# Performance work log

Hardware: AMD Instinct MI355X
Metric: run time of the kernel (lower is better)

## Reference

```python
import jax, jax.numpy as jnp
import numpy as np
from jax import lax

T, B, D_IN, D_DAY, H, D_OUT = 64, 32, 4096, 256, 256, 942


def setup_inputs() -> dict:
    key = jax.random.key(0)
    ks = jax.random.split(key, 18)
    s = 0.05
    def rn(k, shape):
        return jax.random.normal(k, shape, jnp.float32) * s
    return {
        "x": jax.random.uniform(ks[0], (T, B, D_IN), jnp.float32),
        "W_emb": rn(ks[1], (D_DAY, D_IN)), "b_emb": rn(ks[2], (D_DAY,)),
        "Wih_f": rn(ks[3], (3 * H, D_DAY)), "Whh_f": rn(ks[4], (3 * H, H)),
        "bih_f": rn(ks[5], (3 * H,)), "bhh_f": rn(ks[6], (3 * H,)),
        "Wih_r": rn(ks[7], (3 * H, D_DAY)), "Whh_r": rn(ks[8], (3 * H, H)),
        "bih_r": rn(ks[9], (3 * H,)), "bhh_r": rn(ks[10], (3 * H,)),
        "attn_w": rn(ks[11], (2 * H,)), "attn_b": rn(ks[12], ()),
        "W_ao": rn(ks[13], (D_DAY, 4 * H)), "b_ao": rn(ks[14], (D_DAY,)),
        "W_o": rn(ks[15], (D_OUT, D_DAY)), "b_o": rn(ks[16], (D_OUT,)),
    }


def _gru_cell(xt, h, Wih, Whh, bih, bhh):
    # PyTorch nn.GRU cell math
    gi = xt @ Wih.T + bih          # [B, 3H]
    gh = h @ Whh.T + bhh           # [B, 3H]
    ir, iz, inn = jnp.split(gi, 3, axis=-1)
    hr, hz, hn = jnp.split(gh, 3, axis=-1)
    r = jax.nn.sigmoid(ir + hr)
    z = jax.nn.sigmoid(iz + hz)
    n = jnp.tanh(inn + r * hn)
    return (1.0 - z) * n + z * h


def _run_gru(seq, Wih, Whh, bih, bhh):
    # seq: [L, B, D] -> all hidden states [L, B, H], h0 = zeros
    h0 = jnp.zeros((seq.shape[1], H), seq.dtype)
    def step(h, xt):
        h2 = _gru_cell(xt, h, Wih, Whh, bih, bhh)
        return h2, h2
    return lax.scan(step, h0, seq)[1]


def reference(x, W_emb, b_emb, Wih_f, Whh_f, bih_f, bhh_f,
              Wih_r, Whh_r, bih_r, bhh_r, attn_w, attn_b,
              W_ao, b_ao, W_o, b_o):
    day_emb = jnp.einsum('tbi,di->tbd', x, W_emb) + b_emb       # [T,B,Dday]

    # Forward GRU over the prefix [:i+1] equals the first i+1 states of one full run.
    fwd = _run_gru(day_emb, Wih_f, Whh_f, bih_f, bhh_f)          # [T,B,H]

    # Reverse GRU is recomputed per timestep on the flipped prefix (O(T^2)).
    i_idx = jnp.arange(T)
    j_idx = jnp.arange(T)
    gather = jnp.clip(i_idx[:, None] - j_idx[None, :], 0)        # [T,T]
    rev_in = day_emb[gather]                                     # [T,T,B,Dday]; row i, step j = day_emb[i-j]
    rev = jax.vmap(lambda s: _run_gru(s, Wih_r, Whh_r, bih_r, bhh_r))(rev_in)  # [T,T,B,H]

    # Attention scores on concat(fwd, rev) without materializing the 2H concat:
    w_f, w_r = attn_w[:H], attn_w[H:]
    scores = (jnp.einsum('tbh,h->tb', fwd, w_f)[None, :, :]
              + jnp.einsum('itbh,h->itb', rev, w_r) + attn_b)    # [T(i),T(t),B]
    valid = j_idx[None, :] <= i_idx[:, None]                     # t <= i
    scores = jnp.where(valid[:, :, None], scores, -jnp.inf)
    alpha = jax.nn.softmax(scores, axis=1)                       # softmax over prefix time

    counts = (i_idx + 1).astype(day_emb.dtype)[:, None, None]    # mean over i+1 steps
    c_fwd = jnp.einsum('itb,tbh->ibh', alpha, fwd) / counts      # [T,B,H]
    c_rev = jnp.einsum('itb,itbh->ibh', alpha, rev) / counts     # [T,B,H]
    rev_last = rev[i_idx, i_idx]                                 # rnn_h[-1] reverse half, [T,B,H]

    h_t = jnp.concatenate([c_fwd, c_rev, fwd, rev_last], axis=-1)  # [T,B,4H]
    h_t_out = h_t @ W_ao.T + b_ao                                # [T,B,Dday]
    return jax.nn.sigmoid(h_t_out @ W_o.T + b_o)                 # [T,B,D_OUT]
```

## Files before the change

kernel.cpp:

```cpp
#include <hip/hip_runtime.h>
#include <hip/hip_bf16.h>


typedef __bf16 bf16x8 __attribute__((ext_vector_type(8)));
typedef __bf16 bf16x4 __attribute__((ext_vector_type(4)));
typedef float  f32x4  __attribute__((ext_vector_type(4)));
typedef int    int4v  __attribute__((ext_vector_type(4)));

static constexpr float NEG_L2E = -1.442695041f;
static constexpr float TWO_L2E =  2.885390082f;

static constexpr size_t OFF_PK_EMB = 0;
static constexpr size_t OFF_PK_IH  = 2097152;
static constexpr size_t OFF_WQ     = 2883584;
static constexpr size_t OFF_WSC    = 3276800;
static constexpr size_t OFF_PK_AO  = 3670016;
static constexpr size_t OFF_PK_O   = 4194304;
static constexpr size_t OFF_DAY    = 4685824;
static constexpr size_t OFF_GIT    = 5734400;
static constexpr size_t OFF_BC     = 12025856;
static constexpr size_t OFF_REV    = 18317312;
static constexpr size_t OFF_FWD    = 52396032;
static constexpr size_t OFF_HT     = 53444608;
static constexpr size_t OFF_TMP1   = 57638912;
static constexpr size_t OFF_XB     = OFF_REV;

__device__ __forceinline__ float sigf(float x) {
    return __builtin_amdgcn_rcpf(1.f + __expf(-x));
}

#define LDS_BARRIER() asm volatile("s_waitcnt lgkmcnt(0)\n\ts_barrier" ::: "memory")

__global__ __launch_bounds__(256) void pack_misc(
    const float* __restrict__ We,  const float* __restrict__ Wir, const float* __restrict__ Wif,
    const float* __restrict__ Wao, const float* __restrict__ Wo,  const float* __restrict__ x,
    __bf16* pe, __bf16* pi, __bf16* pao, __bf16* po, __bf16* xb)
{
    int b = blockIdx.x;
    if (b >= 952) {
        size_t base = ((size_t)(b - 952) * 256 + threadIdx.x) * 8;
        float4 v0 = *(const float4*)(x + base);
        float4 v1 = *(const float4*)(x + base + 4);
        bf16x8 o;
        o[0]=(__bf16)v0.x; o[1]=(__bf16)v0.y; o[2]=(__bf16)v0.z; o[3]=(__bf16)v0.w;
        o[4]=(__bf16)v1.x; o[5]=(__bf16)v1.y; o[6]=(__bf16)v1.z; o[7]=(__bf16)v1.w;
        *(bf16x8*)(xb + base) = o;
        return;
    }
    const float* src; __bf16* dst; int Nsrc, k32l, b0; bool ih = false;
    if (b < 512)      { src = We;  dst = pe;          Nsrc = 256; k32l = 7; b0 = 0;   }
    else if (b < 608) { src = Wir; dst = pi;          Nsrc = 768; k32l = 3; b0 = 512; ih = true; }
    else if (b < 704) { src = Wif; dst = pi + 196608; Nsrc = 768; k32l = 3; b0 = 608; ih = true; }
    else if (b < 832) { src = Wao; dst = pao;         Nsrc = 256; k32l = 5; b0 = 704; }
    else              { src = Wo;  dst = po;          Nsrc = 942; k32l = 3; b0 = 832; }
    int t8   = (b - b0) * 256 + threadIdx.x;
    int lane = t8 & 63;
    int K32  = 1 << k32l;
    int K    = K32 << 5;
    int ks   = (t8 >> 6) & (K32 - 1);
    int nt   = t8 >> (6 + k32l);
    int n    = nt * 16 + (lane & 15);
    int k0   = ks * 32 + ((lane >> 4) << 3);
    bf16x8 o;
    if (n < Nsrc) {
        const float* sp = src + (size_t)n * K + k0;
        float4 v0 = *(const float4*)sp;
        float4 v1 = *(const float4*)(sp + 4);
        float s = ih ? ((n < 512) ? NEG_L2E : TWO_L2E) : 1.f;
        o[0]=(__bf16)(v0.x*s); o[1]=(__bf16)(v0.y*s); o[2]=(__bf16)(v0.z*s); o[3]=(__bf16)(v0.w*s);
        o[4]=(__bf16)(v1.x*s); o[5]=(__bf16)(v1.y*s); o[6]=(__bf16)(v1.z*s); o[7]=(__bf16)(v1.w*s);
    } else {
#pragma unroll
        for (int q = 0; q < 8; q++) o[q] = (__bf16)0.f;
    }
    *(bf16x8*)(dst + (size_t)t8 * 8) = o;
}

__global__ __launch_bounds__(64) void pack_hh_i8(
    const float* __restrict__ Whr, const float* __restrict__ Whf,
    const float* __restrict__ bih_r, const float* __restrict__ bih_f,
    const float* __restrict__ bhh_r, const float* __restrict__ bhh_f,
    signed char* __restrict__ wq, float* __restrict__ wscale, float* __restrict__ bc)
{
    int b = blockIdx.x;
    int dir = (b >= 768) ? 1 : 0;
    int n = b - dir * 768;
    const float* src = (dir ? Whf : Whr) + (size_t)n * 256;
    int t = threadIdx.x;
    float4 wv = ((const float4*)src)[t];
    float m = fmaxf(fmaxf(fabsf(wv.x), fabsf(wv.y)), fmaxf(fabsf(wv.z), fabsf(wv.w)));
#pragma unroll
    for (int off = 32; off > 0; off >>= 1) m = fmaxf(m, __shfl_xor(m, off));
    m = fmaxf(m, 1e-20f);
    float inv = 127.f / m;
    int q0 = (int)__builtin_rintf(wv.x * inv);
    int q1 = (int)__builtin_rintf(wv.y * inv);
    int q2 = (int)__builtin_rintf(wv.z * inv);
    int q3 = (int)__builtin_rintf(wv.w * inv);
    int pk = (q0 & 0xff) | ((q1 & 0xff) << 8) | ((q2 & 0xff) << 16) | ((q3 & 0xff) << 24);
    int dlane = (n & 15) | (((t >> 2) & 3) << 4);
    size_t byte = (size_t)dir * 196608 + ((size_t)(n >> 4) * 4 + (t >> 4)) * 1024
                + (size_t)dlane * 16 + (t & 3) * 4;
    *(int*)(wq + byte) = pk;
    if (t == 0) {
        float gc = (n < 512) ? NEG_L2E : TWO_L2E;
        wscale[b] = m * (1.f / 16129.f) * gc;
        const float* bi = dir ? bih_f : bih_r;
        const float* bh = dir ? bhh_f : bhh_r;
        bc[b] = (n < 512) ? (bi[n] + bh[n]) * NEG_L2E : bi[n] * TWO_L2E;
    }
}

template<int MODE, int KDIM, int NTILES, int MR, int CSTRIDE, int NREAL>
__global__ __launch_bounds__(256) void gemm_k(
    const __bf16* __restrict__ Ap, const __bf16* __restrict__ Bp, void* __restrict__ Cp,
    const float* __restrict__ bias)
{
    __shared__ __align__(16) __bf16 As[MR][88];
    const int tid = threadIdx.x;
    const int w = tid >> 6, lane = tid & 63, c = lane & 15, quad = lane >> 4;
    const int mb = blockIdx.x, nb = blockIdx.y;
    constexpr int K32 = KDIM / 32;
    constexpr int NK  = KDIM / 64;
    constexpr int NT_W = (MR == 64) ? NTILES : NTILES / 2;
    constexpr int TPR  = (MR == 64) ? 4 : 8;
    constexpr int EPT  = 64 / TPR;
    const int wrow  = (MR == 64) ? w : (w & 1);
    const int ncol0 = (MR == 64) ? 0 : (w >> 1) * NT_W;

    f32x4 acc[NT_W];
#pragma unroll
    for (int nt = 0; nt < NT_W; nt++) acc[nt] = (f32x4){0.f, 0.f, 0.f, 0.f};

    const int row = tid / TPR, kp = (tid % TPR) * EPT;
    uint4 pb[EPT / 8];

    auto issue = [&](int kb) {
        const __bf16* ap = Ap + (size_t)(mb * MR + row) * KDIM + kb * 64 + kp;
        pb[0] = ((const uint4*)ap)[0];
        if constexpr (EPT == 16) pb[1] = ((const uint4*)ap)[1];
    };
    auto commit = [&]() {
        *(uint4*)&As[row][kp] = pb[0];
        if constexpr (EPT == 16) *(uint4*)&As[row][kp + 8] = pb[1];
    };

    issue(0);
    for (int kb = 0; kb < NK; kb++) {
        commit();
        __syncthreads();
        if (kb + 1 < NK) issue(kb + 1);
#pragma unroll
        for (int kk = 0; kk < 2; kk++) {
            bf16x8 a = *(const bf16x8*)&As[wrow * 16 + c][kk * 32 + quad * 8];
#pragma unroll
            for (int nt = 0; nt < NT_W; nt++) {
                bf16x8 bfr = *(const bf16x8*)(Bp +
                    ((size_t)((nb * NTILES + ncol0 + nt) * K32 + kb * 2 + kk) * 64 + lane) * 8);
                acc[nt] = __builtin_amdgcn_mfma_f32_16x16x32_bf16(a, bfr, acc[nt], 0, 0, 0);
            }
        }
        __syncthreads();
    }

    if constexpr (MODE == 1) {
        static_assert(MR == 64 && NTILES == 4, "MODE1 epilogue requires 64x64 tile");
#pragma unroll
        for (int nt = 0; nt < 4; nt++) {
            float bv = bias[nb * 64 + nt * 16 + c];
#pragma unroll
            for (int r0 = 0; r0 < 4; r0++)
                As[nt * 16 + c][w * 16 + quad * 4 + r0] = (__bf16)(acc[nt][r0] + bv);
        }
        __syncthreads();
        const int dd = tid >> 2, bch = tid & 3;
        const int n = nb * 64 + dd;
        const int dir = (n >= 768) ? 1 : 0;
        const int rem = n - dir * 768;
        const int g = rem >> 8, dcol = rem & 255;
#pragma unroll
        for (int tl = 0; tl < 2; tl++) {
            uint4 v = *(const uint4*)&As[dd][tl * 32 + bch * 8];
            size_t off = (size_t)dir * 1572864 + (size_t)(mb * 2 + tl) * 24576
                       + ((size_t)((g * 2 + (bch >> 1)) * 256 + dcol)) * 16 + (bch & 1) * 8;
            *(uint4*)((__bf16*)Cp + off) = v;
        }
    } else {
#pragma unroll
        for (int nt = 0; nt < NT_W; nt++) {
            int n = nb * (NTILES * 16) + (ncol0 + nt) * 16 + c;
            float bv = (n < NREAL) ? bias[n] : 0.f;
#pragma unroll
            for (int r0 = 0; r0 < 4; r0++) {
                int m = mb * MR + wrow * 16 + quad * 4 + r0;
                float v = acc[nt][r0] + bv;
                if constexpr (MODE == 2) ((__bf16*)Cp)[(size_t)m * CSTRIDE + n] = (__bf16)v;
                else { if (n < NREAL) ((float*)Cp)[(size_t)m * CSTRIDE + n] = sigf(v); }
            }
        }
    }
}

__global__ __launch_bounds__(1024, 4) void gru_recurrent(
    const signed char* __restrict__ wq, const float* __restrict__ wscale,
    const float* __restrict__ bhh_r, const float* __restrict__ bhh_f,
    const __bf16* __restrict__ Git,
    __bf16* __restrict__ revb, __bf16* __restrict__ fwdb)
{
    __shared__ __align__(16) signed char hbuf[2][16][272];
    __shared__ __align__(16) __bf16 hist[8][4096];
    const int tid = threadIdx.x;
    const int w = tid >> 6, lane = tid & 63, c = lane & 15, quad = lane >> 4;
    const int bid = blockIdx.x;
    const bool isF = (bid < 2);
    const int ia = isF ? 63 : (63 - ((bid - 2) >> 1));
    const int bh = bid & 1;
    const int b0 = bh << 4;
    const int steps = ia + 1;
    const float* bhh = isF ? bhh_f : bhh_r;
    __bf16* outb = isF ? fwdb : (revb + ((size_t)(ia * (ia + 1) / 2)) * 8192);

    const int4v* pw = (const int4v*)(wq + (isF ? 196608 : 0));
    int4v bw[3][4];
#pragma unroll
    for (int g = 0; g < 3; g++)
#pragma unroll
        for (int ks = 0; ks < 4; ks++)
            bw[g][ks] = pw[(size_t)((g * 16 + w) * 4 + ks) * 64 + lane];
    const int d = (w << 4) + c;
    float sc[3];
#pragma unroll
    for (int g = 0; g < 3; g++) sc[g] = wscale[(isF ? 768 : 0) + g * 256 + d];
    const float bnv = bhh[512 + d] * TWO_L2E;

    float hreg[4] = {0.f, 0.f, 0.f, 0.f};
    for (int idx = tid; idx < 2 * 16 * 272 / 4; idx += 1024) ((int*)hbuf)[idx] = 0;
    __syncthreads();

    const __bf16* gb = Git + (size_t)(isF ? 64 : ia) * 24576;
    const long gstep = isF ? 24576 : -24576;
    int loff[3];
#pragma unroll
    for (int g = 0; g < 3; g++) loff[g] = ((g * 2 + bh) * 256 + d) * 16 + (quad << 2);

    auto flush = [&](int jbase, int cnt) {
        int s = tid >> 7;
        if (s < cnt) {
            const uint4* src = (const uint4*)((const char*)&hist[s][0] + (tid & 127) * 64);
            uint4 v0 = src[0], v1 = src[1], v2 = src[2], v3 = src[3];
            uint4* dst = (uint4*)(outb + (size_t)(jbase + s) * 8192 + b0 * 256 + (tid & 127) * 32);
            dst[0] = v0; dst[1] = v1; dst[2] = v2; dst[3] = v3;
        }
    };

    bf16x4 gcur[3], gnxt[3];
#pragma unroll
    for (int g = 0; g < 3; g++) gcur[g] = *(const bf16x4*)(gb + loff[g]);

    for (int j = 0; j < steps; j++) {
        const int rb = j & 1, wbuf = rb ^ 1;

        if (j + 1 < steps) {
            const __bf16* gn = gb + gstep;
#pragma unroll
            for (int g = 0; g < 3; g++) gnxt[g] = *(const bf16x4*)(gn + loff[g]);
        }

        int4v a0 = {0,0,0,0}, a1 = {0,0,0,0}, a2 = {0,0,0,0};
#pragma unroll
        for (int ks = 0; ks < 4; ks++) {
            int4v av = *(const int4v*)&hbuf[rb][c][ks * 64 + quad * 16];
            a0 = __builtin_amdgcn_mfma_i32_16x16x64_i8(av, bw[0][ks], a0, 0, 0, 0);
            a1 = __builtin_amdgcn_mfma_i32_16x16x64_i8(av, bw[1][ks], a1, 0, 0, 0);
            a2 = __builtin_amdgcn_mfma_i32_16x16x64_i8(av, bw[2][ks], a2, 0, 0, 0);
        }

        const int hs = j & 7;
#pragma unroll
        for (int r0 = 0; r0 < 4; r0++) {
            float er = __builtin_amdgcn_exp2f(fmaf((float)a0[r0], sc[0], (float)gcur[0][r0]));
            float rg = __builtin_amdgcn_rcpf(1.f + er);
            float ez = __builtin_amdgcn_exp2f(fmaf((float)a1[r0], sc[1], (float)gcur[1][r0]));
            float zg = __builtin_amdgcn_rcpf(1.f + ez);
            float narg = fmaf(rg, fmaf((float)a2[r0], sc[2], bnv), (float)gcur[2][r0]);
            float en = __builtin_amdgcn_exp2f(narg);
            float ng = fmaf(-2.f, __builtin_amdgcn_rcpf(1.f + en), 1.f);
            float h  = fmaf(zg, hreg[r0] - ng, ng);
            hreg[r0] = h;
            int row = (quad << 2) + r0;
            hbuf[wbuf][row][d] = (signed char)(int)__builtin_rintf(h * 127.f);
            hist[hs][row * 256 + d] = (__bf16)h;
        }
        LDS_BARRIER();
        if (hs == 7) {
            flush(j - 7, 8);
            LDS_BARRIER();
        }
        gb += gstep;
#pragma unroll
        for (int g = 0; g < 3; g++) gcur[g] = gnxt[g];
    }
    int rem = steps & 7;
    if (rem) flush(steps - rem, rem);
}

__global__ __launch_bounds__(512) void attn_kernel(
    const __bf16* __restrict__ revb, const __bf16* __restrict__ fwdb,
    const float* __restrict__ attn_w, const float* __restrict__ attn_bp,
    __bf16* __restrict__ ht)
{
    const int tid = threadIdx.x;
    const int w = tid >> 6, lane = tid & 63;
    const int wid = blockIdx.x * 8 + w;
    const int i = wid >> 5, b = wid & 31;
    const int d0 = lane * 4;

    float wf[4], wr[4];
#pragma unroll
    for (int q = 0; q < 4; q++) { wf[q] = attn_w[d0 + q]; wr[q] = attn_w[256 + d0 + q]; }
    const float ab = attn_bp[0];
    const __bf16* rp = revb + ((size_t)(i * (i + 1) / 2)) * 8192 + (size_t)b * 256 + d0;
    const __bf16* fp = fwdb + (size_t)b * 256 + d0;

    float mx = -1e30f, l = 0.f;
    float cf[4] = {0,0,0,0}, cr[4] = {0,0,0,0};
    bf16x4 rn = *(const bf16x4*)rp, fn = *(const bf16x4*)fp;
    for (int t = 0; t <= i; t++) {
        bf16x4 rv4 = rn, fv4 = fn;
        if (t < i) {
            rn = *(const bf16x4*)(rp + (size_t)(t + 1) * 8192);
            fn = *(const bf16x4*)(fp + (size_t)(t + 1) * 8192);
        }
        float rv[4], fv[4], s = 0.f;
#pragma unroll
        for (int q = 0; q < 4; q++) {
            rv[q] = (float)rv4[q]; fv[q] = (float)fv4[q];
            s += rv[q] * wr[q] + fv[q] * wf[q];
        }
#pragma unroll
        for (int off = 32; off > 0; off >>= 1) s += __shfl_xor(s, off);
        s += ab;
        float mn = fmaxf(mx, s);
        float scl = __expf(mx - mn);
        float p  = __expf(s - mn);
        l = l * scl + p;
#pragma unroll
        for (int q = 0; q < 4; q++) { cf[q] = cf[q] * scl + p * fv[q]; cr[q] = cr[q] * scl + p * rv[q]; }
        mx = mn;
    }
    float inv = __builtin_amdgcn_rcpf(l * (float)(i + 1));
    __bf16* hp = ht + (size_t)(i * 32 + b) * 1024 + d0;
    const __bf16* fl = fp + (size_t)i * 8192;
    const __bf16* rl = rp + (size_t)i * 8192;
#pragma unroll
    for (int q = 0; q < 4; q++) {
        hp[q]       = (__bf16)(cf[q] * inv);
        hp[256 + q] = (__bf16)(cr[q] * inv);
        hp[512 + q] = fl[q];
        hp[768 + q] = rl[q];
    }
}

extern "C" void kernel_launch(void* const* d_in, const int* in_sizes, int n_in,
                              void* d_out, int out_size, void* d_ws, size_t ws_size,
                              hipStream_t stream) {
    const float* x      = (const float*)d_in[0];
    const float* W_emb  = (const float*)d_in[1];
    const float* b_emb  = (const float*)d_in[2];
    const float* Wih_f  = (const float*)d_in[3];
    const float* Whh_f  = (const float*)d_in[4];
    const float* bih_f  = (const float*)d_in[5];
    const float* bhh_f  = (const float*)d_in[6];
    const float* Wih_r  = (const float*)d_in[7];
    const float* Whh_r  = (const float*)d_in[8];
    const float* bih_r  = (const float*)d_in[9];
    const float* bhh_r  = (const float*)d_in[10];
    const float* attn_w = (const float*)d_in[11];
    const float* attn_b = (const float*)d_in[12];
    const float* W_ao   = (const float*)d_in[13];
    const float* b_ao   = (const float*)d_in[14];
    const float* W_o    = (const float*)d_in[15];
    const float* b_o    = (const float*)d_in[16];
    float* out = (float*)d_out;

    char* ws = (char*)d_ws;
    __bf16* pk_emb = (__bf16*)(ws + OFF_PK_EMB);
    __bf16* pk_ih  = (__bf16*)(ws + OFF_PK_IH);
    signed char* wq = (signed char*)(ws + OFF_WQ);
    float*  wsc    = (float*)(ws + OFF_WSC);
    __bf16* pk_ao  = (__bf16*)(ws + OFF_PK_AO);
    __bf16* pk_o   = (__bf16*)(ws + OFF_PK_O);
    __bf16* day    = (__bf16*)(ws + OFF_DAY);
    __bf16* Git    = (__bf16*)(ws + OFF_GIT);
    float*  bc     = (float*)(ws + OFF_BC);
    __bf16* revb   = (__bf16*)(ws + OFF_REV);
    __bf16* fwdb   = (__bf16*)(ws + OFF_FWD);
    __bf16* ht     = (__bf16*)(ws + OFF_HT);
    __bf16* tmp1   = (__bf16*)(ws + OFF_TMP1);
    __bf16* xb     = (__bf16*)(ws + OFF_XB);

    pack_misc<<<5048, 256, 0, stream>>>(W_emb, Wih_r, Wih_f, W_ao, W_o, x,
                                        pk_emb, pk_ih, pk_ao, pk_o, xb);
    pack_hh_i8<<<1536, 64, 0, stream>>>(Whh_r, Whh_f, bih_r, bih_f, bhh_r, bhh_f,
                                        wq, wsc, bc);

    gemm_k<2, 4096, 4, 32, 256, 256><<<dim3(64, 4), 256, 0, stream>>>(xb, pk_emb, day, b_emb);
    gemm_k<1, 256, 4, 64, 1536, 1536><<<dim3(32, 24), 256, 0, stream>>>(day, pk_ih, Git, bc);

    gru_recurrent<<<130, 1024, 0, stream>>>(wq, wsc, bhh_r, bhh_f, Git, revb, fwdb);

    attn_kernel<<<256, 512, 0, stream>>>(revb, fwdb, attn_w, attn_b, ht);

    gemm_k<2, 1024, 4, 32, 256, 256><<<dim3(64, 4), 256, 0, stream>>>(ht, pk_ao, tmp1, b_ao);
    gemm_k<3, 256, 4, 32, 942, 942><<<dim3(64, 15), 256, 0, stream>>>(tmp1, pk_o, out, b_o);
}
```

Baseline: 350.0 us.

## Fuse output head GEMMs, merge int8 packing into pack_misc, prefetch B fragments

Merges the int8 recurrent-weight quantization kernel into pack_misc as extra blocks, removing one launch. Splits the GEMM template into a specialized embedding GEMM and a Git GEMM, both now double-buffering B fragments in registers. Fuses the two output-head GEMMs (W_ao then W_o with sigmoid) into one kernel that keeps the intermediate in LDS, dropping the tmp1 round trip and one launch. The fused head uses only 64 blocks with a large accumulator set, so parallelism and register pressure may limit it.

```diff
diff --git a/kernel.cpp b/kernel.cpp
--- a/kernel.cpp
+++ b/kernel.cpp
@@ -22,7 +22,6 @@
 static constexpr size_t OFF_REV    = 18317312;
 static constexpr size_t OFF_FWD    = 52396032;
 static constexpr size_t OFF_HT     = 53444608;
-static constexpr size_t OFF_TMP1   = 57638912;
 static constexpr size_t OFF_XB     = OFF_REV;
 
 __device__ __forceinline__ float sigf(float x) {
@@ -34,9 +33,43 @@
 __global__ __launch_bounds__(256) void pack_misc(
     const float* __restrict__ We,  const float* __restrict__ Wir, const float* __restrict__ Wif,
     const float* __restrict__ Wao, const float* __restrict__ Wo,  const float* __restrict__ x,
-    __bf16* pe, __bf16* pi, __bf16* pao, __bf16* po, __bf16* xb)
+    const float* __restrict__ Whr, const float* __restrict__ Whf,
+    const float* __restrict__ bih_r, const float* __restrict__ bih_f,
+    const float* __restrict__ bhh_r, const float* __restrict__ bhh_f,
+    __bf16* pe, __bf16* pi, __bf16* pao, __bf16* po, __bf16* xb,
+    signed char* __restrict__ wq, float* __restrict__ wscale, float* __restrict__ bc)
 {
     int b = blockIdx.x;
+    if (b >= 5048) {
+        int rowb = (b - 5048) * 4 + (threadIdx.x >> 6);
+        int t = threadIdx.x & 63;
+        int dir = (rowb >= 768) ? 1 : 0;
+        int n = rowb - dir * 768;
+        const float* src = (dir ? Whf : Whr) + (size_t)n * 256;
+        float4 wv = ((const float4*)src)[t];
+        float m = fmaxf(fmaxf(fabsf(wv.x), fabsf(wv.y)), fmaxf(fabsf(wv.z), fabsf(wv.w)));
+#pragma unroll
+        for (int off = 32; off > 0; off >>= 1) m = fmaxf(m, __shfl_xor(m, off));
+        m = fmaxf(m, 1e-20f);
+        float inv = 127.f / m;
+        int q0 = (int)__builtin_rintf(wv.x * inv);
+        int q1 = (int)__builtin_rintf(wv.y * inv);
+        int q2 = (int)__builtin_rintf(wv.z * inv);
+        int q3 = (int)__builtin_rintf(wv.w * inv);
+        int pk = (q0 & 0xff) | ((q1 & 0xff) << 8) | ((q2 & 0xff) << 16) | ((q3 & 0xff) << 24);
+        int dlane = (n & 15) | (((t >> 2) & 3) << 4);
+        size_t byte = (size_t)dir * 196608 + ((size_t)(n >> 4) * 4 + (t >> 4)) * 1024
+                    + (size_t)dlane * 16 + (t & 3) * 4;
+        *(int*)(wq + byte) = pk;
+        if (t == 0) {
+            float gc = (n < 512) ? NEG_L2E : TWO_L2E;
+            wscale[rowb] = m * (1.f / 16129.f) * gc;
+            const float* bi = dir ? bih_f : bih_r;
+            const float* bh = dir ? bhh_f : bhh_r;
+            bc[rowb] = (n < 512) ? (bi[n] + bh[n]) * NEG_L2E : bi[n] * TWO_L2E;
+        }
+        return;
+    }
     if (b >= 952) {
         size_t base = ((size_t)(b - 952) * 256 + threadIdx.x) * 8;
         float4 v0 = *(const float4*)(x + base);
@@ -76,128 +109,147 @@
     *(bf16x8*)(dst + (size_t)t8 * 8) = o;
 }
 
-__global__ __launch_bounds__(64) void pack_hh_i8(
-    const float* __restrict__ Whr, const float* __restrict__ Whf,
-    const float* __restrict__ bih_r, const float* __restrict__ bih_f,
-    const float* __restrict__ bhh_r, const float* __restrict__ bhh_f,
-    signed char* __restrict__ wq, float* __restrict__ wscale, float* __restrict__ bc)
-{
-    int b = blockIdx.x;
-    int dir = (b >= 768) ? 1 : 0;
-    int n = b - dir * 768;
-    const float* src = (dir ? Whf : Whr) + (size_t)n * 256;
-    int t = threadIdx.x;
-    float4 wv = ((const float4*)src)[t];
-    float m = fmaxf(fmaxf(fabsf(wv.x), fabsf(wv.y)), fmaxf(fabsf(wv.z), fabsf(wv.w)));
-#pragma unroll
-    for (int off = 32; off > 0; off >>= 1) m = fmaxf(m, __shfl_xor(m, off));
-    m = fmaxf(m, 1e-20f);
-    float inv = 127.f / m;
-    int q0 = (int)__builtin_rintf(wv.x * inv);
-    int q1 = (int)__builtin_rintf(wv.y * inv);
-    int q2 = (int)__builtin_rintf(wv.z * inv);
-    int q3 = (int)__builtin_rintf(wv.w * inv);
-    int pk = (q0 & 0xff) | ((q1 & 0xff) << 8) | ((q2 & 0xff) << 16) | ((q3 & 0xff) << 24);
-    int dlane = (n & 15) | (((t >> 2) & 3) << 4);
-    size_t byte = (size_t)dir * 196608 + ((size_t)(n >> 4) * 4 + (t >> 4)) * 1024
-                + (size_t)dlane * 16 + (t & 3) * 4;
-    *(int*)(wq + byte) = pk;
-    if (t == 0) {
-        float gc = (n < 512) ? NEG_L2E : TWO_L2E;
-        wscale[b] = m * (1.f / 16129.f) * gc;
-        const float* bi = dir ? bih_f : bih_r;
-        const float* bh = dir ? bhh_f : bhh_r;
-        bc[b] = (n < 512) ? (bi[n] + bh[n]) * NEG_L2E : bi[n] * TWO_L2E;
-    }
-}
-
-template<int MODE, int KDIM, int NTILES, int MR, int CSTRIDE, int NREAL>
+template<int KDIM, int NTILES, int CSTRIDE>
 __global__ __launch_bounds__(256) void gemm_k(
-    const __bf16* __restrict__ Ap, const __bf16* __restrict__ Bp, void* __restrict__ Cp,
+    const __bf16* __restrict__ Ap, const __bf16* __restrict__ Bp, __bf16* __restrict__ Cp,
     const float* __restrict__ bias)
 {
-    __shared__ __align__(16) __bf16 As[MR][88];
+    __shared__ __align__(16) __bf16 As[32][88];
     const int tid = threadIdx.x;
     const int w = tid >> 6, lane = tid & 63, c = lane & 15, quad = lane >> 4;
     const int mb = blockIdx.x, nb = blockIdx.y;
     constexpr int K32 = KDIM / 32;
     constexpr int NK  = KDIM / 64;
-    constexpr int NT_W = (MR == 64) ? NTILES : NTILES / 2;
-    constexpr int TPR  = (MR == 64) ? 4 : 8;
-    constexpr int EPT  = 64 / TPR;
-    const int wrow  = (MR == 64) ? w : (w & 1);
-    const int ncol0 = (MR == 64) ? 0 : (w >> 1) * NT_W;
+    constexpr int NT_W = NTILES / 2;
+    const int wrow = w & 1, ncol0 = (w >> 1) * NT_W;
 
     f32x4 acc[NT_W];
 #pragma unroll
     for (int nt = 0; nt < NT_W; nt++) acc[nt] = (f32x4){0.f, 0.f, 0.f, 0.f};
 
-    const int row = tid / TPR, kp = (tid % TPR) * EPT;
-    uint4 pb[EPT / 8];
-
-    auto issue = [&](int kb) {
-        const __bf16* ap = Ap + (size_t)(mb * MR + row) * KDIM + kb * 64 + kp;
-        pb[0] = ((const uint4*)ap)[0];
-        if constexpr (EPT == 16) pb[1] = ((const uint4*)ap)[1];
+    const int row = tid >> 3, kp = (tid & 7) * 8;
+    uint4 pb;
+    auto issue  = [&](int kb) { pb = *(const uint4*)(Ap + (size_t)(mb * 32 + row) * KDIM + kb * 64 + kp); };
+    auto commit = [&]() { *(uint4*)&As[row][kp] = pb; };
+
+    bf16x8 bcur[2][NT_W], bnxt[2][NT_W];
+    auto loadB = [&](int kb, bf16x8 (&dst)[2][NT_W]) {
+#pragma unroll
+        for (int kk = 0; kk < 2; kk++)
+#pragma unroll
+            for (int nt = 0; nt < NT_W; nt++)
+                dst[kk][nt] = *(const bf16x8*)(Bp +
+                    ((size_t)((nb * NTILES + ncol0 + nt) * K32 + kb * 2 + kk) * 64 + lane) * 8);
     };
-    auto commit = [&]() {
-        *(uint4*)&As[row][kp] = pb[0];
-        if constexpr (EPT == 16) *(uint4*)&As[row][kp + 8] = pb[1];
-    };
 
     issue(0);
+    loadB(0, bcur);
     for (int kb = 0; kb < NK; kb++) {
         commit();
         __syncthreads();
-        if (kb + 1 < NK) issue(kb + 1);
+        if (kb + 1 < NK) { issue(kb + 1); loadB(kb + 1, bnxt); }
 #pragma unroll
         for (int kk = 0; kk < 2; kk++) {
             bf16x8 a = *(const bf16x8*)&As[wrow * 16 + c][kk * 32 + quad * 8];
 #pragma unroll
-            for (int nt = 0; nt < NT_W; nt++) {
-                bf16x8 bfr = *(const bf16x8*)(Bp +
-                    ((size_t)((nb * NTILES + ncol0 + nt) * K32 + kb * 2 + kk) * 64 + lane) * 8);
-                acc[nt] = __builtin_amdgcn_mfma_f32_16x16x32_bf16(a, bfr, acc[nt], 0, 0, 0);
-            }
+            for (int nt = 0; nt < NT_W; nt++)
+                acc[nt] = __builtin_amdgcn_mfma_f32_16x16x32_bf16(a, bcur[kk][nt], acc[nt], 0, 0, 0);
+        }
+        if (kb + 1 < NK) {
+#pragma unroll
+            for (int kk = 0; kk < 2; kk++)
+#pragma unroll
+                for (int nt = 0; nt < NT_W; nt++) bcur[kk][nt] = bnxt[kk][nt];
         }
         __syncthreads();
     }
 
-    if constexpr (MODE == 1) {
-        static_assert(MR == 64 && NTILES == 4, "MODE1 epilogue requires 64x64 tile");
-#pragma unroll
-        for (int nt = 0; nt < 4; nt++) {
-            float bv = bias[nb * 64 + nt * 16 + c];
-#pragma unroll
-            for (int r0 = 0; r0 < 4; r0++)
-                As[nt * 16 + c][w * 16 + quad * 4 + r0] = (__bf16)(acc[nt][r0] + bv);
-        }
+#pragma unroll
+    for (int nt = 0; nt < NT_W; nt++) {
+        int n = nb * (NTILES * 16) + (ncol0 + nt) * 16 + c;
+        float bv = bias[n];
+#pragma unroll
+        for (int r0 = 0; r0 < 4; r0++) {
+            int m = mb * 32 + wrow * 16 + quad * 4 + r0;
+            Cp[(size_t)m * CSTRIDE + n] = (__bf16)(acc[nt][r0] + bv);
+        }
+    }
+}
+
+__global__ __launch_bounds__(256) void gemm_git(
+    const __bf16* __restrict__ Ap, const __bf16* __restrict__ Bp, __bf16* __restrict__ Cp,
+    const float* __restrict__ bias)
+{
+    __shared__ __align__(16) __bf16 As[64][88];
+    const int tid = threadIdx.x;
+    const int w = tid >> 6, lane = tid & 63, c = lane & 15, quad = lane >> 4;
+    const int mb = blockIdx.x, nb = blockIdx.y;
+
+    f32x4 acc[4];
+#pragma unroll
+    for (int nt = 0; nt < 4; nt++) acc[nt] = (f32x4){0.f, 0.f, 0.f, 0.f};
+
+    const int row = tid >> 2, kp = (tid & 3) * 16;
+    uint4 pb[2];
+    auto issue = [&](int kb) {
+        const __bf16* ap = Ap + (size_t)(mb * 64 + row) * 256 + kb * 64 + kp;
+        pb[0] = ((const uint4*)ap)[0]; pb[1] = ((const uint4*)ap)[1];
+    };
+    auto commit = [&]() {
+        *(uint4*)&As[row][kp] = pb[0]; *(uint4*)&As[row][kp + 8] = pb[1];
+    };
+
+    bf16x8 bcur[2][4], bnxt[2][4];
+    auto loadB = [&](int kb, bf16x8 (&dst)[2][4]) {
+#pragma unroll
+        for (int kk = 0; kk < 2; kk++)
+#pragma unroll
+            for (int nt = 0; nt < 4; nt++)
+                dst[kk][nt] = *(const bf16x8*)(Bp +
+                    ((size_t)((nb * 4 + nt) * 8 + kb * 2 + kk) * 64 + lane) * 8);
+    };
+
+    issue(0);
+    loadB(0, bcur);
+    for (int kb = 0; kb < 4; kb++) {
+        commit();
         __syncthreads();
-        const int dd = tid >> 2, bch = tid & 3;
-        const int n = nb * 64 + dd;
-        const int dir = (n >= 768) ? 1 : 0;
-        const int rem = n - dir * 768;
-        const int g = rem >> 8, dcol = rem & 255;
-#pragma unroll
-        for (int tl = 0; tl < 2; tl++) {
-            uint4 v = *(const uint4*)&As[dd][tl * 32 + bch * 8];
-            size_t off = (size_t)dir * 1572864 + (size_t)(mb * 2 + tl) * 24576
-                       + ((size_t)((g * 2 + (bch >> 1)) * 256 + dcol)) * 16 + (bch & 1) * 8;
-            *(uint4*)((__bf16*)Cp + off) = v;
-        }
-    } else {
-#pragma unroll
-        for (int nt = 0; nt < NT_W; nt++) {
-            int n = nb * (NTILES * 16) + (ncol0 + nt) * 16 + c;
-            float bv = (n < NREAL) ? bias[n] : 0.f;
-#pragma unroll
-            for (int r0 = 0; r0 < 4; r0++) {
-                int m = mb * MR + wrow * 16 + quad * 4 + r0;
-                float v = acc[nt][r0] + bv;
-                if constexpr (MODE == 2) ((__bf16*)Cp)[(size_t)m * CSTRIDE + n] = (__bf16)v;
-                else { if (n < NREAL) ((float*)Cp)[(size_t)m * CSTRIDE + n] = sigf(v); }
-            }
-        }
+        if (kb + 1 < 4) { issue(kb + 1); loadB(kb + 1, bnxt); }
+#pragma unroll
+        for (int kk = 0; kk < 2; kk++) {
+            bf16x8 a = *(const bf16x8*)&As[w * 16 + c][kk * 32 + quad * 8];
+#pragma unroll
+            for (int nt = 0; nt < 4; nt++)
+                acc[nt] = __builtin_amdgcn_mfma_f32_16x16x32_bf16(a, bcur[kk][nt], acc[nt], 0, 0, 0);
+        }
+        if (kb + 1 < 4) {
+#pragma unroll
+            for (int kk = 0; kk < 2; kk++)
+#pragma unroll
+                for (int nt = 0; nt < 4; nt++) bcur[kk][nt] = bnxt[kk][nt];
+        }
+        __syncthreads();
+    }
+
+#pragma unroll
+    for (int nt = 0; nt < 4; nt++) {
+        float bv = bias[nb * 64 + nt * 16 + c];
+#pragma unroll
+        for (int r0 = 0; r0 < 4; r0++)
+            As[nt * 16 + c][w * 16 + quad * 4 + r0] = (__bf16)(acc[nt][r0] + bv);
+    }
+    __syncthreads();
+    const int dd = tid >> 2, bch = tid & 3;
+    const int n = nb * 64 + dd;
+    const int dir = (n >= 768) ? 1 : 0;
+    const int rem = n - dir * 768;
+    const int g = rem >> 8, dcol = rem & 255;
+#pragma unroll
+    for (int tl = 0; tl < 2; tl++) {
+        uint4 v = *(const uint4*)&As[dd][tl * 32 + bch * 8];
+        size_t off = (size_t)dir * 1572864 + (size_t)(mb * 2 + tl) * 24576
+                   + ((size_t)((g * 2 + (bch >> 1)) * 256 + dcol)) * 16 + (bch & 1) * 8;
+        *(uint4*)(Cp + off) = v;
     }
 }
 
@@ -269,7 +321,7 @@
         int4v a0 = {0,0,0,0}, a1 = {0,0,0,0}, a2 = {0,0,0,0};
 #pragma unroll
         for (int ks = 0; ks < 4; ks++) {
-            int4v av = *(const int4v*)&hbuf[rb][c][ks * 64 + quad * 16];
+            int4v av = *(const int4v*)&hbuf[rb][c][ks * 64 + (quad << 4)];
             a0 = __builtin_amdgcn_mfma_i32_16x16x64_i8(av, bw[0][ks], a0, 0, 0, 0);
             a1 = __builtin_amdgcn_mfma_i32_16x16x64_i8(av, bw[1][ks], a1, 0, 0, 0);
             a2 = __builtin_amdgcn_mfma_i32_16x16x64_i8(av, bw[2][ks], a2, 0, 0, 0);
@@ -358,6 +410,88 @@
         hp[256 + q] = (__bf16)(cr[q] * inv);
         hp[512 + q] = fl[q];
         hp[768 + q] = rl[q];
+    }
+}
+
+__global__ __launch_bounds__(256, 1) void head_fused(
+    const __bf16* __restrict__ ht, const __bf16* __restrict__ Bao, const float* __restrict__ bao,
+    const __bf16* __restrict__ Bo, const float* __restrict__ bo, float* __restrict__ out)
+{
+    __shared__ __align__(16) __bf16 As[32][88];
+    __shared__ __align__(16) __bf16 tmp[32][264];
+    const int tid = threadIdx.x;
+    const int w = tid >> 6, lane = tid & 63, c = lane & 15, quad = lane >> 4;
+    const int mb = blockIdx.x;
+
+    const int wrow = w & 1, colg = w >> 1;
+    f32x4 acc1[8];
+#pragma unroll
+    for (int nt = 0; nt < 8; nt++) acc1[nt] = (f32x4){0.f, 0.f, 0.f, 0.f};
+    const int row = tid >> 3, kp = (tid & 7) * 8;
+    uint4 pb;
+    auto issue  = [&](int kb) { pb = *(const uint4*)(ht + (size_t)(mb * 32 + row) * 1024 + kb * 64 + kp); };
+    auto commit = [&]() { *(uint4*)&As[row][kp] = pb; };
+
+    issue(0);
+    for (int kb = 0; kb < 16; kb++) {
+        commit();
+        __syncthreads();
+        if (kb + 1 < 16) issue(kb + 1);
+#pragma unroll
+        for (int kk = 0; kk < 2; kk++) {
+            bf16x8 a = *(const bf16x8*)&As[wrow * 16 + c][kk * 32 + quad * 8];
+#pragma unroll
+            for (int nt = 0; nt < 8; nt++) {
+                bf16x8 bfr = *(const bf16x8*)(Bao +
+                    ((size_t)((colg * 8 + nt) * 32 + kb * 2 + kk) * 64 + lane) * 8);
+                acc1[nt] = __builtin_amdgcn_mfma_f32_16x16x32_bf16(a, bfr, acc1[nt], 0, 0, 0);
+            }
+        }
+        __syncthreads();
+    }
+#pragma unroll
+    for (int nt = 0; nt < 8; nt++) {
+        int n = colg * 128 + nt * 16 + c;
+        float bv = bao[n];
+#pragma unroll
+        for (int r0 = 0; r0 < 4; r0++)
+            tmp[wrow * 16 + quad * 4 + r0][n] = (__bf16)(acc1[nt][r0] + bv);
+    }
+    __syncthreads();
+
+    f32x4 acc2[2][15];
+#pragma unroll
+    for (int rt = 0; rt < 2; rt++)
+#pragma unroll
+        for (int nt = 0; nt < 15; nt++) acc2[rt][nt] = (f32x4){0.f, 0.f, 0.f, 0.f};
+#pragma unroll
+    for (int kb = 0; kb < 4; kb++) {
+#pragma unroll
+        for (int kk = 0; kk < 2; kk++) {
+            bf16x8 a0 = *(const bf16x8*)&tmp[c][kb * 64 + kk * 32 + quad * 8];
+            bf16x8 a1 = *(const bf16x8*)&tmp[16 + c][kb * 64 + kk * 32 + quad * 8];
+#pragma unroll
+            for (int nt = 0; nt < 15; nt++) {
+                bf16x8 bfr = *(const bf16x8*)(Bo +
+                    ((size_t)((w * 15 + nt) * 8 + kb * 2 + kk) * 64 + lane) * 8);
+                acc2[0][nt] = __builtin_amdgcn_mfma_f32_16x16x32_bf16(a0, bfr, acc2[0][nt], 0, 0, 0);
+                acc2[1][nt] = __builtin_amdgcn_mfma_f32_16x16x32_bf16(a1, bfr, acc2[1][nt], 0, 0, 0);
+            }
+        }
+    }
+#pragma unroll
+    for (int nt = 0; nt < 15; nt++) {
+        int n = (w * 15 + nt) * 16 + c;
+        if (n < 942) {
+            float bv = bo[n];
+#pragma unroll
+            for (int rt = 0; rt < 2; rt++)
+#pragma unroll
+                for (int r0 = 0; r0 < 4; r0++) {
+                    int m = mb * 32 + rt * 16 + quad * 4 + r0;
+                    out[(size_t)m * 942 + n] = sigf(acc2[rt][nt][r0] + bv);
+                }
+        }
     }
 }
 
@@ -396,21 +530,18 @@
     __bf16* revb   = (__bf16*)(ws + OFF_REV);
     __bf16* fwdb   = (__bf16*)(ws + OFF_FWD);
     __bf16* ht     = (__bf16*)(ws + OFF_HT);
-    __bf16* tmp1   = (__bf16*)(ws + OFF_TMP1);
     __bf16* xb     = (__bf16*)(ws + OFF_XB);
 
-    pack_misc<<<5048, 256, 0, stream>>>(W_emb, Wih_r, Wih_f, W_ao, W_o, x,
-                                        pk_emb, pk_ih, pk_ao, pk_o, xb);
-    pack_hh_i8<<<1536, 64, 0, stream>>>(Whh_r, Whh_f, bih_r, bih_f, bhh_r, bhh_f,
-                                        wq, wsc, bc);
-
-    gemm_k<2, 4096, 4, 32, 256, 256><<<dim3(64, 4), 256, 0, stream>>>(xb, pk_emb, day, b_emb);
-    gemm_k<1, 256, 4, 64, 1536, 1536><<<dim3(32, 24), 256, 0, stream>>>(day, pk_ih, Git, bc);
+    pack_misc<<<5432, 256, 0, stream>>>(W_emb, Wih_r, Wih_f, W_ao, W_o, x,
+                                        Whh_r, Whh_f, bih_r, bih_f, bhh_r, bhh_f,
+                                        pk_emb, pk_ih, pk_ao, pk_o, xb, wq, wsc, bc);
+
+    gemm_k<4096, 4, 256><<<dim3(64, 4), 256, 0, stream>>>(xb, pk_emb, day, b_emb);
+    gemm_git<<<dim3(32, 24), 256, 0, stream>>>(day, pk_ih, Git, bc);
 
     gru_recurrent<<<130, 1024, 0, stream>>>(wq, wsc, bhh_r, bhh_f, Git, revb, fwdb);
 
     attn_kernel<<<256, 512, 0, stream>>>(revb, fwdb, attn_w, attn_b, ht);
 
-    gemm_k<2, 1024, 4, 32, 256, 256><<<dim3(64, 4), 256, 0, stream>>>(ht, pk_ao, tmp1, b_ao);
-    gemm_k<3, 256, 4, 32, 942, 942><<<dim3(64, 15), 256, 0, stream>>>(tmp1, pk_o, out, b_o);
-}
+    head_fused<<<64, 256, 0, stream>>>(ht, pk_ao, b_ao, pk_o, b_o, out);
+}
```

After: 383.6 us. 9.6% more time.
